# Kernel optimization log

Measured on AMD Instinct MI355X. Metric: run time of the kernel, lower is better.

Reference implementation:

```python
import jax, jax.numpy as jnp
import numpy as np

EMBED = 1024
HEADS = 16
HEAD_DIM = EMBED // HEADS
OUT_DIM = 1024


def setup_inputs() -> dict:
    key = jax.random.key(0)
    ks = jax.random.split(key, 8)
    N, L = 2, 2048
    values = jax.random.normal(ks[0], (N, L, EMBED), dtype=jnp.float32)
    keys_t = jax.random.normal(ks[1], (N, L, EMBED), dtype=jnp.float32)
    query = jax.random.normal(ks[2], (N, L, EMBED), dtype=jnp.float32)
    s = 1.0 / np.sqrt(HEAD_DIM)
    Wv = jax.random.normal(ks[3], (HEAD_DIM, HEAD_DIM), dtype=jnp.float32) * s
    Wk = jax.random.normal(ks[4], (HEAD_DIM, HEAD_DIM), dtype=jnp.float32) * s
    Wq = jax.random.normal(ks[5], (HEAD_DIM, HEAD_DIM), dtype=jnp.float32) * s
    Wout = jax.random.normal(ks[6], (OUT_DIM, EMBED), dtype=jnp.float32) * (1.0 / np.sqrt(EMBED))
    bout = jax.random.normal(ks[7], (OUT_DIM,), dtype=jnp.float32) * 0.01
    return {"values": values, "keys": keys_t, "query": query,
            "Wv": Wv, "Wk": Wk, "Wq": Wq, "Wout": Wout, "bout": bout}


def reference(values, keys, query, Wv, Wk, Wq, Wout, bout):
    N, Lq, _ = query.shape
    Lk = keys.shape[1]
    # split into heads: (N, L, H, D)
    v = values.reshape(N, Lk, HEADS, HEAD_DIM)
    k = keys.reshape(N, Lk, HEADS, HEAD_DIM)
    q = query.reshape(N, Lq, HEADS, HEAD_DIM)
    # per-head shared linear projections (torch Linear: x @ W.T, no bias)
    v = jnp.einsum('nlhd,ed->nlhe', v, Wv)
    k = jnp.einsum('nlhd,ed->nlhe', k, Wk)
    q = jnp.einsum('nqhd,ed->nqhe', q, Wq)
    # scores (N, H, Q, K); NOTE: scale is 1/sqrt(embed_size), per original code
    scores = jnp.einsum('nqhd,nkhd->nhqk', q, k) / jnp.sqrt(jnp.float32(EMBED))
    attn = jax.nn.softmax(scores, axis=-1)
    out = jnp.einsum('nhqk,nkhd->nqhd', attn, v).reshape(N, Lq, EMBED)
    # fc_out: x @ Wout.T + bout
    return out @ Wout.T + bout
```

## Files before the change

### kernel.cpp

```cpp
#include <hip/hip_runtime.h>
#include <cstdint>

typedef __attribute__((ext_vector_type(8))) short short8;
typedef __attribute__((ext_vector_type(4))) float floatx4;
typedef __attribute__((ext_vector_type(4))) _Float16 half4;
typedef __attribute__((ext_vector_type(2))) __fp16 fp16x2;

#define DEV __device__ __forceinline__

constexpr int NB = 2, Lseq = 2048, NH = 16, HD = 64, EMB = 1024;
constexpr float QSCALE = 0.03125f * 1.4426950408889634f;

DEV uint16_t f2bf(float f) {
  uint32_t x = __builtin_bit_cast(uint32_t, f);
  x += 0x7fffu + ((x >> 16) & 1u);
  return (uint16_t)(x >> 16);
}

DEV uint32_t pack2(float lo, float hi) {
  uint32_t a = __builtin_bit_cast(uint32_t, lo) + 0x8000u;
  uint32_t b = __builtin_bit_cast(uint32_t, hi) + 0x8000u;
  return __builtin_amdgcn_perm(b, a, 0x07060302);
}

DEV uint32_t packh2(float lo, float hi) {
  return __builtin_bit_cast(uint32_t, __builtin_amdgcn_cvt_pkrtz(lo, hi));
}

DEV void gl_lds16(const void* g, void* l) {
  __builtin_amdgcn_global_load_lds((const __attribute__((address_space(1))) void*)g,
                                   (__attribute__((address_space(3))) void*)l, 16, 0, 0);
}

DEV short8 ld8bf(const float* p, float sc) {
  float4 u = *(const float4*)p;
  float4 v = *(const float4*)(p + 4);
  union { short8 s; uint32_t d[4]; } r;
  r.d[0] = pack2(u.x * sc, u.y * sc);
  r.d[1] = pack2(u.z * sc, u.w * sc);
  r.d[2] = pack2(v.x * sc, v.y * sc);
  r.d[3] = pack2(v.z * sc, v.w * sc);
  return r.s;
}

__global__ __launch_bounds__(256) void prep_kernel(
    const float* __restrict__ values, const float* __restrict__ keysrc,
    const float* __restrict__ query, const float* __restrict__ Wv,
    const float* __restrict__ Wk, const float* __restrict__ Wq,
    const float* __restrict__ Wout,
    uint16_t* __restrict__ qp, uint16_t* __restrict__ kp,
    uint16_t* __restrict__ vp, uint16_t* __restrict__ wbf) {
  const int t = threadIdx.x, w = t >> 6, lane = t & 63;
  const int quad = lane >> 4, l16 = lane & 15;
  const int wid = blockIdx.x * 4 + w;
  const int mat = wid >> 10, sub = wid & 1023;

  if (mat == 3) {
#pragma unroll
    for (int i = 0; i < 4; ++i) {
      int idx = sub * 256 + i * 64 + lane;
      float4 v = ((const float4*)Wout)[idx];
      uint2 p;
      p.x = pack2(v.x, v.y);
      p.y = pack2(v.z, v.w);
      ((uint2*)wbf)[idx] = p;
    }
    return;
  }

  floatx4 c[4][4];
#pragma unroll
  for (int i = 0; i < 4; ++i)
#pragma unroll
    for (int j = 0; j < 4; ++j) c[i][j] = floatx4{0.f, 0.f, 0.f, 0.f};

  if (mat < 2) {
    const float* src = mat ? keysrc : query;
    const float* W   = mat ? Wk : Wq;
    const float asc  = mat ? 1.f : QSCALE;
    uint16_t* dst    = mat ? kp : qp;
    const int R0 = sub * 64;
    short8 a[4][2], b[4][2];
#pragma unroll
    for (int dc = 0; dc < 2; ++dc) {
#pragma unroll
      for (int f = 0; f < 4; ++f) {
        a[f][dc] = ld8bf(W + (size_t)(f * 16 + l16) * 64 + dc * 32 + quad * 8, asc);
        b[f][dc] = ld8bf(src + (size_t)(R0 + f * 16 + l16) * 64 + dc * 32 + quad * 8, 1.f);
      }
    }
#pragma unroll
    for (int dc = 0; dc < 2; ++dc)
#pragma unroll
      for (int mf = 0; mf < 4; ++mf)
#pragma unroll
        for (int nf = 0; nf < 4; ++nf)
          c[mf][nf] = __builtin_amdgcn_mfma_f32_16x16x32_bf16(a[mf][dc], b[nf][dc], c[mf][nf], 0, 0, 0);
#pragma unroll
    for (int nf = 0; nf < 4; ++nf) {
      int r = R0 + nf * 16 + l16;
      int h = r & 15, l = (r >> 4) & 2047, n = r >> 15;
      uint16_t* drow = dst + ((size_t)(n * 16 + h) * 2048 + l) * 64;
#pragma unroll
      for (int mf = 0; mf < 4; ++mf) {
        uint2 pk;
        pk.x = pack2(c[mf][nf][0], c[mf][nf][1]);
        pk.y = pack2(c[mf][nf][2], c[mf][nf][3]);
        *(uint2*)(drow + mf * 16 + quad * 4) = pk;
      }
    }
  } else {
    const int nh = sub >> 5, L0 = (sub & 31) * 64;
    const int n = nh >> 4, h = nh & 15;
    short8 a[4][2], b[4][2];
#pragma unroll
    for (int dc = 0; dc < 2; ++dc) {
#pragma unroll
      for (int f = 0; f < 4; ++f) {
        a[f][dc] = ld8bf(values + (size_t)(n * 2048 + L0 + f * 16 + l16) * 1024 + h * 64 + dc * 32 + quad * 8, 1.f);
        b[f][dc] = ld8bf(Wv + (size_t)(f * 16 + l16) * 64 + dc * 32 + quad * 8, 1.f);
      }
    }
#pragma unroll
    for (int dc = 0; dc < 2; ++dc)
#pragma unroll
      for (int mf = 0; mf < 4; ++mf)
#pragma unroll
        for (int nf = 0; nf < 4; ++nf)
          c[mf][nf] = __builtin_amdgcn_mfma_f32_16x16x32_bf16(a[mf][dc], b[nf][dc], c[mf][nf], 0, 0, 0);
#pragma unroll
    for (int nf = 0; nf < 4; ++nf) {
      int d = nf * 16 + l16;
      uint16_t* drow = vp + ((size_t)nh * 64 + d) * 2048 + L0;
#pragma unroll
      for (int mf = 0; mf < 4; ++mf) {
        uint2 pk;
        pk.x = packh2(c[mf][nf][0], c[mf][nf][1]);
        pk.y = packh2(c[mf][nf][2], c[mf][nf][3]);
        *(uint2*)(drow + mf * 16 + quad * 4) = pk;
      }
    }
  }
}

__global__ __launch_bounds__(256, 3) void flash_kernel(const uint16_t* __restrict__ qp,
                                                       const uint16_t* __restrict__ kp,
                                                       const uint16_t* __restrict__ vp,
                                                       uint16_t* __restrict__ xatt,
                                                       float* __restrict__ opart,
                                                       float* __restrict__ psum_g,
                                                       int kbn) {
  __shared__ uint16_t Kt[2][64 * 64];
  __shared__ uint16_t Vt[2][64 * 64];
  const int t = threadIdx.x;
  const int w = t >> 6, lane = t & 63, quad = lane >> 4, l16 = lane & 15;
  const int nh = blockIdx.y, qt = blockIdx.x, kh = blockIdx.z;
  const int q0 = qt * 128 + w * 32;
  const uint16_t* Qb = qp + (size_t)nh * Lseq * HD;
  const uint16_t* Kb = kp + (size_t)nh * Lseq * HD + (size_t)kh * kbn * 64 * 64;
  const uint16_t* Vb = vp + (size_t)nh * HD * Lseq;
  const int vcol0 = kh * kbn * 64;
  const int srow = lane >> 3, sc8 = (lane & 7) ^ (lane >> 3);

  short8 bq[2][2];
#pragma unroll
  for (int qb = 0; qb < 2; ++qb) {
    bq[qb][0] = *(const short8*)(Qb + (q0 + qb * 16 + l16) * 64 + quad * 8);
    bq[qb][1] = *(const short8*)(Qb + (q0 + qb * 16 + l16) * 64 + 32 + quad * 8);
  }

  floatx4 o[4][2];
  float psum[2] = {0.f, 0.f};
#pragma unroll
  for (int i = 0; i < 4; ++i)
#pragma unroll
    for (int qb = 0; qb < 2; ++qb) o[i][qb] = floatx4{0.f, 0.f, 0.f, 0.f};

#pragma unroll
  for (int i = 0; i < 2; ++i) {
    int r0 = w * 16 + i * 8;
    gl_lds16(Kb + (r0 + srow) * 64 + sc8 * 8, &Kt[0][r0 * 64]);
    gl_lds16(Vb + (size_t)(r0 + srow) * Lseq + vcol0 + sc8 * 8, &Vt[0][r0 * 64]);
  }

  for (int kb = 0; kb < kbn; ++kb) {
    __syncthreads();
    const int cur = kb & 1;
    if (kb + 1 < kbn) {
      const int nxt = cur ^ 1;
      const uint16_t* kg = Kb + (kb + 1) * (64 * 64);
#pragma unroll
      for (int i = 0; i < 2; ++i) {
        int r0 = w * 16 + i * 8;
        gl_lds16(kg + (r0 + srow) * 64 + sc8 * 8, &Kt[nxt][r0 * 64]);
        gl_lds16(Vb + (size_t)(r0 + srow) * Lseq + vcol0 + (kb + 1) * 64 + sc8 * 8, &Vt[nxt][r0 * 64]);
      }
    }

    floatx4 s[4][2];
#pragma unroll
    for (int kb16 = 0; kb16 < 4; ++kb16)
#pragma unroll
      for (int qb = 0; qb < 2; ++qb) s[kb16][qb] = floatx4{0.f, 0.f, 0.f, 0.f};
#pragma unroll
    for (int dc = 0; dc < 2; ++dc) {
#pragma unroll
      for (int kb16 = 0; kb16 < 4; ++kb16) {
        int row = kb16 * 16 + l16;
        short8 ak = *(const short8*)(&Kt[cur][row * 64 + ((dc * 4 + quad) ^ (row & 7)) * 8]);
        s[kb16][0] = __builtin_amdgcn_mfma_f32_16x16x32_bf16(ak, bq[0][dc], s[kb16][0], 0, 0, 0);
        s[kb16][1] = __builtin_amdgcn_mfma_f32_16x16x32_bf16(ak, bq[1][dc], s[kb16][1], 0, 0, 0);
      }
    }

    half4 bp[4][2];
#pragma unroll
    for (int qb = 0; qb < 2; ++qb) {
#pragma unroll
      for (int kb16 = 0; kb16 < 4; ++kb16) {
        float p0 = __builtin_amdgcn_exp2f(s[kb16][qb][0]);
        float p1 = __builtin_amdgcn_exp2f(s[kb16][qb][1]);
        float p2 = __builtin_amdgcn_exp2f(s[kb16][qb][2]);
        float p3 = __builtin_amdgcn_exp2f(s[kb16][qb][3]);
        psum[qb] += (p0 + p1) + (p2 + p3);
        union { half4 h4; uint32_t d[2]; } u;
        u.d[0] = packh2(p0, p1);
        u.d[1] = packh2(p2, p3);
        bp[kb16][qb] = u.h4;
      }
    }

#pragma unroll
    for (int kb16 = 0; kb16 < 4; ++kb16) {
#pragma unroll
      for (int db = 0; db < 4; ++db) {
        int row = db * 16 + l16;
        int ch = (kb16 * 2 + (quad >> 1)) ^ (row & 7);
        half4 av = *(const half4*)(&Vt[cur][row * 64 + ch * 8 + (quad & 1) * 4]);
        o[db][0] = __builtin_amdgcn_mfma_f32_16x16x16f16(av, bp[kb16][0], o[db][0], 0, 0, 0);
        o[db][1] = __builtin_amdgcn_mfma_f32_16x16x16f16(av, bp[kb16][1], o[db][1], 0, 0, 0);
      }
    }
  }

  if (opart) {
    float* ob = opart + (((size_t)nh * 16 + qt) * 2 + kh) * 8192 + (size_t)w * 8 * 256;
#pragma unroll
    for (int db = 0; db < 4; ++db)
#pragma unroll
      for (int qb = 0; qb < 2; ++qb)
        *(floatx4*)(ob + (db * 2 + qb) * 256 + lane * 4) = o[db][qb];
#pragma unroll
    for (int qb = 0; qb < 2; ++qb) {
      float l = psum[qb];
      l += __shfl_xor(l, 16, 64);
      l += __shfl_xor(l, 32, 64);
      if (quad == 0)
        psum_g[(((size_t)nh * 16 + qt) * 2 + kh) * 128 + w * 32 + qb * 16 + l16] = l;
    }
  } else {
    const int n = nh >> 4, h = nh & 15;
#pragma unroll
    for (int qb = 0; qb < 2; ++qb) {
      float l = psum[qb];
      l += __shfl_xor(l, 16, 64);
      l += __shfl_xor(l, 32, 64);
      float inv = 1.f / l;
      size_t rowb = (size_t)(n * Lseq + q0 + qb * 16 + l16) * EMB + h * 64;
#pragma unroll
      for (int db = 0; db < 4; ++db) {
        uint2 pk;
        pk.x = pack2(o[db][qb][0] * inv, o[db][qb][1] * inv);
        pk.y = pack2(o[db][qb][2] * inv, o[db][qb][3] * inv);
        *(uint2*)(xatt + rowb + db * 16 + quad * 4) = pk;
      }
    }
  }
}

__global__ __launch_bounds__(256) void combine_kernel(const float* __restrict__ opart,
                                                      const float* __restrict__ psum_g,
                                                      uint16_t* __restrict__ xatt) {
  const int t = threadIdx.x, w = t >> 6, lane = t & 63, quad = lane >> 4, l16 = lane & 15;
  const int qt = blockIdx.x, nh = blockIdx.y;
  const int n = nh >> 4, h = nh & 15;
  const size_t tb = ((size_t)nh * 16 + qt) * 2;
  const float* oa = opart + tb * 8192 + (size_t)w * 8 * 256;
  const float* ob = opart + (tb + 1) * 8192 + (size_t)w * 8 * 256;
  float inv[2];
#pragma unroll
  for (int qb = 0; qb < 2; ++qb) {
    int q = w * 32 + qb * 16 + l16;
    inv[qb] = 1.f / (psum_g[tb * 128 + q] + psum_g[(tb + 1) * 128 + q]);
  }
#pragma unroll
  for (int db = 0; db < 4; ++db)
#pragma unroll
    for (int qb = 0; qb < 2; ++qb) {
      floatx4 a = *(const floatx4*)(oa + (db * 2 + qb) * 256 + lane * 4);
      floatx4 b = *(const floatx4*)(ob + (db * 2 + qb) * 256 + lane * 4);
      float v0 = (a[0] + b[0]) * inv[qb];
      float v1 = (a[1] + b[1]) * inv[qb];
      float v2 = (a[2] + b[2]) * inv[qb];
      float v3 = (a[3] + b[3]) * inv[qb];
      uint2 pk;
      pk.x = pack2(v0, v1);
      pk.y = pack2(v2, v3);
      size_t row = (size_t)(n * Lseq + qt * 128 + w * 32 + qb * 16 + l16) * EMB + h * 64;
      *(uint2*)(xatt + row + db * 16 + quad * 4) = pk;
    }
}

__global__ __launch_bounds__(256) void gemm_out_kernel(const uint16_t* __restrict__ X,
                                                       const uint16_t* __restrict__ Wb,
                                                       const float* __restrict__ bias,
                                                       float* __restrict__ out) {
  __shared__ uint16_t Xt[2][128 * 64];
  __shared__ uint16_t Wt[2][64 * 64];
  const int t = threadIdx.x, w = t >> 6, lane = t & 63, quad = lane >> 4, l16 = lane & 15;
  const int m0 = blockIdx.y * 128, o0 = blockIdx.x * 64;
  const int srow = lane >> 3, sc8 = (lane & 7) ^ (lane >> 3);
  floatx4 c[2][4];
#pragma unroll
  for (int i = 0; i < 2; ++i)
#pragma unroll
    for (int j = 0; j < 4; ++j) c[i][j] = floatx4{0.f, 0.f, 0.f, 0.f};

#pragma unroll
  for (int i = 0; i < 4; ++i) {
    int r0 = w * 32 + i * 8;
    gl_lds16(X + (size_t)(m0 + r0 + srow) * 1024 + sc8 * 8, &Xt[0][r0 * 64]);
  }
#pragma unroll
  for (int i = 0; i < 2; ++i) {
    int r0 = w * 16 + i * 8;
    gl_lds16(Wb + (size_t)(o0 + r0 + srow) * 1024 + sc8 * 8, &Wt[0][r0 * 64]);
  }

  for (int kt = 0; kt < 16; ++kt) {
    __syncthreads();
    const int cur = kt & 1;
    if (kt + 1 < 16) {
      const int nxt = cur ^ 1;
      const int e0 = (kt + 1) * 64;
#pragma unroll
      for (int i = 0; i < 4; ++i) {
        int r0 = w * 32 + i * 8;
        gl_lds16(X + (size_t)(m0 + r0 + srow) * 1024 + e0 + sc8 * 8, &Xt[nxt][r0 * 64]);
      }
#pragma unroll
      for (int i = 0; i < 2; ++i) {
        int r0 = w * 16 + i * 8;
        gl_lds16(Wb + (size_t)(o0 + r0 + srow) * 1024 + e0 + sc8 * 8, &Wt[nxt][r0 * 64]);
      }
    }
#pragma unroll
    for (int kc = 0; kc < 2; ++kc) {
      short8 a[2], b[4];
#pragma unroll
      for (int mf = 0; mf < 2; ++mf) {
        int row = w * 32 + mf * 16 + l16;
        a[mf] = *(const short8*)(&Xt[cur][row * 64 + ((kc * 4 + quad) ^ (row & 7)) * 8]);
      }
#pragma unroll
      for (int nf = 0; nf < 4; ++nf) {
        int rw = nf * 16 + l16;
        b[nf] = *(const short8*)(&Wt[cur][rw * 64 + ((kc * 4 + quad) ^ (rw & 7)) * 8]);
      }
#pragma unroll
      for (int mf = 0; mf < 2; ++mf)
#pragma unroll
        for (int nf = 0; nf < 4; ++nf)
          c[mf][nf] = __builtin_amdgcn_mfma_f32_16x16x32_bf16(a[mf], b[nf], c[mf][nf], 0, 0, 0);
    }
  }
#pragma unroll
  for (int nf = 0; nf < 4; ++nf) {
    float bv = bias[o0 + nf * 16 + l16];
#pragma unroll
    for (int mf = 0; mf < 2; ++mf)
#pragma unroll
      for (int r = 0; r < 4; ++r)
        out[(size_t)(m0 + w * 32 + mf * 16 + quad * 4 + r) * 1024 + o0 + nf * 16 + l16] =
            c[mf][nf][r] + bv;
  }
}

extern "C" void kernel_launch(void* const* d_in, const int* in_sizes, int n_in,
                              void* d_out, int out_size, void* d_ws, size_t ws_size,
                              hipStream_t stream) {
  const float* values = (const float*)d_in[0];
  const float* keys   = (const float*)d_in[1];
  const float* query  = (const float*)d_in[2];
  const float* Wv     = (const float*)d_in[3];
  const float* Wk     = (const float*)d_in[4];
  const float* Wq     = (const float*)d_in[5];
  const float* Wout   = (const float*)d_in[6];
  const float* bout   = (const float*)d_in[7];
  float* out = (float*)d_out;

  uint16_t* ws  = (uint16_t*)d_ws;
  uint16_t* qp  = ws;
  uint16_t* kp  = ws + (size_t)4194304;
  uint16_t* vp  = ws + (size_t)2 * 4194304;
  uint16_t* xat = ws + (size_t)3 * 4194304;
  uint16_t* wbf = ws + (size_t)4 * 4194304;
  float* opart  = (float*)(ws + (size_t)17825792);
  float* psum   = opart + (size_t)8388608;
  const bool split = ws_size >= 69730304ull;

  prep_kernel<<<dim3(1024), dim3(256), 0, stream>>>(values, keys, query, Wv, Wk, Wq, Wout,
                                                    qp, kp, vp, wbf);
  if (split) {
    flash_kernel<<<dim3(16, 32, 2), dim3(256), 0, stream>>>(qp, kp, vp, nullptr, opart, psum, 16);
    combine_kernel<<<dim3(16, 32), dim3(256), 0, stream>>>(opart, psum, xat);
  } else {
    flash_kernel<<<dim3(16, 32, 1), dim3(256), 0, stream>>>(qp, kp, vp, xat, nullptr, nullptr, 32);
  }
  gemm_out_kernel<<<dim3(16, 32), dim3(256), 0, stream>>>(xat, wbf, bout, out);
}
```

Baseline: 183.2 us.

## Fuse split-K combine into output GEMM and compute row sums via MFMA

Removes the separate combine kernel: the output GEMM now reads the two fp32 partial attention outputs and their row sums, normalizes them and packs to bf16 straight into LDS as the A operand, with W tiles widened to 128 columns. The flash kernel always uses the two-way key split, computes softmax denominators with an extra MFMA against a ones vector instead of scalar adds and shuffles, raises occupancy to 4, and swaps grid axes. This avoids one launch and a bf16 round-trip through global memory, at the cost of the GEMM re-reading fp32 partials eight times (once per output block column), more register pressure, and dropping the non-split fallback path.

```diff
diff --git a/kernel.cpp b/kernel.cpp
--- a/kernel.cpp
+++ b/kernel.cpp
@@ -4,7 +4,6 @@
 typedef __attribute__((ext_vector_type(8))) short short8;
 typedef __attribute__((ext_vector_type(4))) float floatx4;
 typedef __attribute__((ext_vector_type(4))) _Float16 half4;
-typedef __attribute__((ext_vector_type(2))) __fp16 fp16x2;
 
 #define DEV __device__ __forceinline__
 
@@ -143,18 +142,17 @@
   }
 }
 
-__global__ __launch_bounds__(256, 3) void flash_kernel(const uint16_t* __restrict__ qp,
+__global__ __launch_bounds__(256, 4) void flash_kernel(const uint16_t* __restrict__ qp,
                                                        const uint16_t* __restrict__ kp,
                                                        const uint16_t* __restrict__ vp,
-                                                       uint16_t* __restrict__ xatt,
                                                        float* __restrict__ opart,
-                                                       float* __restrict__ psum_g,
-                                                       int kbn) {
+                                                       float* __restrict__ psum_g) {
+  constexpr int kbn = 16;
   __shared__ uint16_t Kt[2][64 * 64];
   __shared__ uint16_t Vt[2][64 * 64];
   const int t = threadIdx.x;
   const int w = t >> 6, lane = t & 63, quad = lane >> 4, l16 = lane & 15;
-  const int nh = blockIdx.y, qt = blockIdx.x, kh = blockIdx.z;
+  const int nh = blockIdx.x, qt = blockIdx.y, kh = blockIdx.z;
   const int q0 = qt * 128 + w * 32;
   const uint16_t* Qb = qp + (size_t)nh * Lseq * HD;
   const uint16_t* Kb = kp + (size_t)nh * Lseq * HD + (size_t)kh * kbn * 64 * 64;
@@ -170,11 +168,14 @@
   }
 
   floatx4 o[4][2];
-  float psum[2] = {0.f, 0.f};
+  floatx4 lfr[2];
 #pragma unroll
   for (int i = 0; i < 4; ++i)
 #pragma unroll
     for (int qb = 0; qb < 2; ++qb) o[i][qb] = floatx4{0.f, 0.f, 0.f, 0.f};
+  lfr[0] = lfr[1] = floatx4{0.f, 0.f, 0.f, 0.f};
+  const _Float16 one = (_Float16)1.0f;
+  const half4 vone = {one, one, one, one};
 
 #pragma unroll
   for (int i = 0; i < 2; ++i) {
@@ -222,12 +223,16 @@
         float p1 = __builtin_amdgcn_exp2f(s[kb16][qb][1]);
         float p2 = __builtin_amdgcn_exp2f(s[kb16][qb][2]);
         float p3 = __builtin_amdgcn_exp2f(s[kb16][qb][3]);
-        psum[qb] += (p0 + p1) + (p2 + p3);
         union { half4 h4; uint32_t d[2]; } u;
         u.d[0] = packh2(p0, p1);
         u.d[1] = packh2(p2, p3);
         bp[kb16][qb] = u.h4;
       }
+    }
+#pragma unroll
+    for (int kb16 = 0; kb16 < 4; ++kb16) {
+      lfr[0] = __builtin_amdgcn_mfma_f32_16x16x16f16(vone, bp[kb16][0], lfr[0], 0, 0, 0);
+      lfr[1] = __builtin_amdgcn_mfma_f32_16x16x16f16(vone, bp[kb16][1], lfr[1], 0, 0, 0);
     }
 
 #pragma unroll
@@ -243,146 +248,128 @@
     }
   }
 
-  if (opart) {
-    float* ob = opart + (((size_t)nh * 16 + qt) * 2 + kh) * 8192 + (size_t)w * 8 * 256;
+  float* ob = opart + (((size_t)nh * 16 + qt) * 2 + kh) * 8192 + (size_t)w * 8 * 256;
+#pragma unroll
+  for (int db = 0; db < 4; ++db)
+#pragma unroll
+    for (int qb = 0; qb < 2; ++qb)
+      *(floatx4*)(ob + (db * 2 + qb) * 256 + lane * 4) = o[db][qb];
+  if (quad == 0) {
+#pragma unroll
+    for (int qb = 0; qb < 2; ++qb)
+      psum_g[(((size_t)nh * 16 + qt) * 2 + kh) * 128 + w * 32 + qb * 16 + l16] = lfr[qb][0];
+  }
+}
+
+__global__ __launch_bounds__(256, 1) void gemm_fused(const float* __restrict__ opart,
+                                                     const float* __restrict__ psum_g,
+                                                     const uint16_t* __restrict__ Wb,
+                                                     const float* __restrict__ bias,
+                                                     float* __restrict__ out) {
+  __shared__ uint16_t Xt[2][128 * 64];
+  __shared__ uint16_t Wt[2][128 * 64];
+  const int t = threadIdx.x, w = t >> 6, lane = t & 63, quad = lane >> 4, l16 = lane & 15;
+  const int mblk = blockIdx.x, obk = blockIdx.y;
+  const int n = mblk >> 4, qt = mblk & 15;
+  const int m0 = mblk * 128, o0 = obk * 128;
+  const int srow = lane >> 3, sc8 = (lane & 7) ^ (lane >> 3);
+
+  floatx4 acc[2][8];
+#pragma unroll
+  for (int i = 0; i < 2; ++i)
+#pragma unroll
+    for (int j = 0; j < 8; ++j) acc[i][j] = floatx4{0.f, 0.f, 0.f, 0.f};
+
+  floatx4 fa[4][2], fb[4][2];
+  float la[2], lb[2];
+
+  auto issue_loads = [&](int h) {
+    size_t tb = ((size_t)(n * 16 + h) * 16 + qt) * 2;
+    const float* pa = opart + tb * 8192 + (size_t)w * 2048 + lane * 4;
 #pragma unroll
     for (int db = 0; db < 4; ++db)
 #pragma unroll
-      for (int qb = 0; qb < 2; ++qb)
-        *(floatx4*)(ob + (db * 2 + qb) * 256 + lane * 4) = o[db][qb];
+      for (int qb = 0; qb < 2; ++qb) {
+        fa[db][qb] = *(const floatx4*)(pa + (db * 2 + qb) * 256);
+        fb[db][qb] = *(const floatx4*)(pa + 8192 + (db * 2 + qb) * 256);
+      }
 #pragma unroll
     for (int qb = 0; qb < 2; ++qb) {
-      float l = psum[qb];
-      l += __shfl_xor(l, 16, 64);
-      l += __shfl_xor(l, 32, 64);
-      if (quad == 0)
-        psum_g[(((size_t)nh * 16 + qt) * 2 + kh) * 128 + w * 32 + qb * 16 + l16] = l;
-    }
-  } else {
-    const int n = nh >> 4, h = nh & 15;
+      la[qb] = psum_g[tb * 128 + w * 32 + qb * 16 + l16];
+      lb[qb] = psum_g[tb * 128 + 128 + w * 32 + qb * 16 + l16];
+    }
+  };
+
+  auto pack_write = [&](int buf) {
 #pragma unroll
     for (int qb = 0; qb < 2; ++qb) {
-      float l = psum[qb];
-      l += __shfl_xor(l, 16, 64);
-      l += __shfl_xor(l, 32, 64);
-      float inv = 1.f / l;
-      size_t rowb = (size_t)(n * Lseq + q0 + qb * 16 + l16) * EMB + h * 64;
+      float inv = __builtin_amdgcn_rcpf(la[qb] + lb[qb]);
+      int q = w * 32 + qb * 16 + l16;
 #pragma unroll
       for (int db = 0; db < 4; ++db) {
+        float v0 = (fa[db][qb][0] + fb[db][qb][0]) * inv;
+        float v1 = (fa[db][qb][1] + fb[db][qb][1]) * inv;
+        float v2 = (fa[db][qb][2] + fb[db][qb][2]) * inv;
+        float v3 = (fa[db][qb][3] + fb[db][qb][3]) * inv;
+        int ch = (db * 2 + (quad >> 1)) ^ (q & 7);
         uint2 pk;
-        pk.x = pack2(o[db][qb][0] * inv, o[db][qb][1] * inv);
-        pk.y = pack2(o[db][qb][2] * inv, o[db][qb][3] * inv);
-        *(uint2*)(xatt + rowb + db * 16 + quad * 4) = pk;
-      }
-    }
-  }
-}
-
-__global__ __launch_bounds__(256) void combine_kernel(const float* __restrict__ opart,
-                                                      const float* __restrict__ psum_g,
-                                                      uint16_t* __restrict__ xatt) {
-  const int t = threadIdx.x, w = t >> 6, lane = t & 63, quad = lane >> 4, l16 = lane & 15;
-  const int qt = blockIdx.x, nh = blockIdx.y;
-  const int n = nh >> 4, h = nh & 15;
-  const size_t tb = ((size_t)nh * 16 + qt) * 2;
-  const float* oa = opart + tb * 8192 + (size_t)w * 8 * 256;
-  const float* ob = opart + (tb + 1) * 8192 + (size_t)w * 8 * 256;
-  float inv[2];
-#pragma unroll
-  for (int qb = 0; qb < 2; ++qb) {
-    int q = w * 32 + qb * 16 + l16;
-    inv[qb] = 1.f / (psum_g[tb * 128 + q] + psum_g[(tb + 1) * 128 + q]);
-  }
-#pragma unroll
-  for (int db = 0; db < 4; ++db)
-#pragma unroll
-    for (int qb = 0; qb < 2; ++qb) {
-      floatx4 a = *(const floatx4*)(oa + (db * 2 + qb) * 256 + lane * 4);
-      floatx4 b = *(const floatx4*)(ob + (db * 2 + qb) * 256 + lane * 4);
-      float v0 = (a[0] + b[0]) * inv[qb];
-      float v1 = (a[1] + b[1]) * inv[qb];
-      float v2 = (a[2] + b[2]) * inv[qb];
-      float v3 = (a[3] + b[3]) * inv[qb];
-      uint2 pk;
-      pk.x = pack2(v0, v1);
-      pk.y = pack2(v2, v3);
-      size_t row = (size_t)(n * Lseq + qt * 128 + w * 32 + qb * 16 + l16) * EMB + h * 64;
-      *(uint2*)(xatt + row + db * 16 + quad * 4) = pk;
-    }
-}
-
-__global__ __launch_bounds__(256) void gemm_out_kernel(const uint16_t* __restrict__ X,
-                                                       const uint16_t* __restrict__ Wb,
-                                                       const float* __restrict__ bias,
-                                                       float* __restrict__ out) {
-  __shared__ uint16_t Xt[2][128 * 64];
-  __shared__ uint16_t Wt[2][64 * 64];
-  const int t = threadIdx.x, w = t >> 6, lane = t & 63, quad = lane >> 4, l16 = lane & 15;
-  const int m0 = blockIdx.y * 128, o0 = blockIdx.x * 64;
-  const int srow = lane >> 3, sc8 = (lane & 7) ^ (lane >> 3);
-  floatx4 c[2][4];
-#pragma unroll
-  for (int i = 0; i < 2; ++i)
-#pragma unroll
-    for (int j = 0; j < 4; ++j) c[i][j] = floatx4{0.f, 0.f, 0.f, 0.f};
-
-#pragma unroll
-  for (int i = 0; i < 4; ++i) {
-    int r0 = w * 32 + i * 8;
-    gl_lds16(X + (size_t)(m0 + r0 + srow) * 1024 + sc8 * 8, &Xt[0][r0 * 64]);
-  }
-#pragma unroll
-  for (int i = 0; i < 2; ++i) {
-    int r0 = w * 16 + i * 8;
-    gl_lds16(Wb + (size_t)(o0 + r0 + srow) * 1024 + sc8 * 8, &Wt[0][r0 * 64]);
-  }
+        pk.x = pack2(v0, v1);
+        pk.y = pack2(v2, v3);
+        *(uint2*)(&Xt[buf][q * 64 + ch * 8 + (quad & 1) * 4]) = pk;
+      }
+    }
+  };
+
+  auto dma_w = [&](int buf, int kt) {
+#pragma unroll
+    for (int i = 0; i < 4; ++i) {
+      int r0 = w * 32 + i * 8;
+      gl_lds16(Wb + (size_t)(o0 + r0 + srow) * 1024 + kt * 64 + sc8 * 8, &Wt[buf][r0 * 64]);
+    }
+  };
+
+  issue_loads(0);
+  pack_write(0);
+  dma_w(0, 0);
 
   for (int kt = 0; kt < 16; ++kt) {
+    const int cur = kt & 1;
     __syncthreads();
-    const int cur = kt & 1;
     if (kt + 1 < 16) {
-      const int nxt = cur ^ 1;
-      const int e0 = (kt + 1) * 64;
-#pragma unroll
-      for (int i = 0; i < 4; ++i) {
-        int r0 = w * 32 + i * 8;
-        gl_lds16(X + (size_t)(m0 + r0 + srow) * 1024 + e0 + sc8 * 8, &Xt[nxt][r0 * 64]);
-      }
-#pragma unroll
-      for (int i = 0; i < 2; ++i) {
-        int r0 = w * 16 + i * 8;
-        gl_lds16(Wb + (size_t)(o0 + r0 + srow) * 1024 + e0 + sc8 * 8, &Wt[nxt][r0 * 64]);
-      }
+      issue_loads(kt + 1);
+      dma_w(cur ^ 1, kt + 1);
     }
 #pragma unroll
     for (int kc = 0; kc < 2; ++kc) {
-      short8 a[2], b[4];
+      short8 a[2], b[8];
 #pragma unroll
       for (int mf = 0; mf < 2; ++mf) {
-        int row = w * 32 + mf * 16 + l16;
-        a[mf] = *(const short8*)(&Xt[cur][row * 64 + ((kc * 4 + quad) ^ (row & 7)) * 8]);
-      }
-#pragma unroll
-      for (int nf = 0; nf < 4; ++nf) {
-        int rw = nf * 16 + l16;
-        b[nf] = *(const short8*)(&Wt[cur][rw * 64 + ((kc * 4 + quad) ^ (rw & 7)) * 8]);
+        int ra = w * 32 + mf * 16 + l16;
+        a[mf] = *(const short8*)(&Xt[cur][ra * 64 + ((kc * 4 + quad) ^ (ra & 7)) * 8]);
+      }
+#pragma unroll
+      for (int nf = 0; nf < 8; ++nf) {
+        int rb = nf * 16 + l16;
+        b[nf] = *(const short8*)(&Wt[cur][rb * 64 + ((kc * 4 + quad) ^ (rb & 7)) * 8]);
       }
 #pragma unroll
       for (int mf = 0; mf < 2; ++mf)
 #pragma unroll
-        for (int nf = 0; nf < 4; ++nf)
-          c[mf][nf] = __builtin_amdgcn_mfma_f32_16x16x32_bf16(a[mf], b[nf], c[mf][nf], 0, 0, 0);
-    }
-  }
-#pragma unroll
-  for (int nf = 0; nf < 4; ++nf) {
+        for (int nf = 0; nf < 8; ++nf)
+          acc[mf][nf] = __builtin_amdgcn_mfma_f32_16x16x32_bf16(a[mf], b[nf], acc[mf][nf], 0, 0, 0);
+    }
+    if (kt + 1 < 16) pack_write(cur ^ 1);
+  }
+
+#pragma unroll
+  for (int nf = 0; nf < 8; ++nf) {
     float bv = bias[o0 + nf * 16 + l16];
 #pragma unroll
     for (int mf = 0; mf < 2; ++mf)
 #pragma unroll
       for (int r = 0; r < 4; ++r)
         out[(size_t)(m0 + w * 32 + mf * 16 + quad * 4 + r) * 1024 + o0 + nf * 16 + l16] =
-            c[mf][nf][r] + bv;
+            acc[mf][nf][r] + bv;
   }
 }
 
@@ -398,24 +385,18 @@
   const float* Wout   = (const float*)d_in[6];
   const float* bout   = (const float*)d_in[7];
   float* out = (float*)d_out;
+  (void)ws_size;
 
   uint16_t* ws  = (uint16_t*)d_ws;
   uint16_t* qp  = ws;
   uint16_t* kp  = ws + (size_t)4194304;
-  uint16_t* vp  = ws + (size_t)2 * 4194304;
-  uint16_t* xat = ws + (size_t)3 * 4194304;
-  uint16_t* wbf = ws + (size_t)4 * 4194304;
-  float* opart  = (float*)(ws + (size_t)17825792);
+  uint16_t* vp  = ws + (size_t)8388608;
+  uint16_t* wbf = ws + (size_t)12582912;
+  float* opart  = (float*)(ws + (size_t)13631488);
   float* psum   = opart + (size_t)8388608;
-  const bool split = ws_size >= 69730304ull;
 
   prep_kernel<<<dim3(1024), dim3(256), 0, stream>>>(values, keys, query, Wv, Wk, Wq, Wout,
                                                     qp, kp, vp, wbf);
-  if (split) {
-    flash_kernel<<<dim3(16, 32, 2), dim3(256), 0, stream>>>(qp, kp, vp, nullptr, opart, psum, 16);
-    combine_kernel<<<dim3(16, 32), dim3(256), 0, stream>>>(opart, psum, xat);
-  } else {
-    flash_kernel<<<dim3(16, 32, 1), dim3(256), 0, stream>>>(qp, kp, vp, xat, nullptr, nullptr, 32);
-  }
-  gemm_out_kernel<<<dim3(16, 32), dim3(256), 0, stream>>>(xat, wbf, bout, out);
-}
+  flash_kernel<<<dim3(32, 16, 2), dim3(256), 0, stream>>>(qp, kp, vp, opart, psum);
+  gemm_fused<<<dim3(32, 8), dim3(256), 0, stream>>>(opart, psum, wbf, bout, out);
+}
```

Result: slower. 189.3 us (+3.4%).
